# Performance work log

Measured on AMD Instinct MI355X. Metric: run time of the kernel, lower is better.

## Reference

```python
import jax, jax.numpy as jnp
import numpy as np

N, T, E, D, U = 32, 2048, 512, 1024, 256


def setup_inputs() -> dict:
    key = jax.random.key(0)
    ks = jax.random.split(key, 6)
    queries = jax.random.normal(ks[0], (N, 1, D), dtype=jnp.float32)
    prev = jax.random.uniform(ks[1], (N, T), dtype=jnp.float32)
    prev = prev / jnp.sum(prev, axis=1, keepdims=True)  # distribution-like initial alignment
    memory = jax.random.normal(ks[2], (N, T, E), dtype=jnp.float32)
    W_q = jax.random.normal(ks[3], (D, U), dtype=jnp.float32) * (1.0 / np.sqrt(D))
    W_k = jax.random.normal(ks[4], (E, U), dtype=jnp.float32) * (1.0 / np.sqrt(E))
    v = jax.random.uniform(ks[5], (U,), dtype=jnp.float32)
    return {"queries": queries, "previous_alignments": prev, "memory": memory,
            "W_q": W_q, "W_k": W_k, "v": v}


def safe_cumprod_exclusive(x):
    # exclusive cumprod via log-space cumsum, clamped like the torch original
    logsum = jnp.cumsum(jnp.log(jnp.clip(x, 1e-20, 1.0)), axis=1)  # [N,T]
    excl = jnp.concatenate([jnp.zeros_like(logsum[:, :1]), logsum], axis=1)[:, :-1]
    return jnp.exp(excl)


def reference(queries, previous_alignments, memory, W_q, W_k, v):
    # Bahdanau additive score (normalize=False path)
    proj_key = jnp.einsum('bte,eu->btu', memory, W_k)          # set_memory
    proj_q = jnp.einsum('bqd,du->bqu', queries, W_q)           # [N,1,U]
    weights = jnp.einsum('btu,u->bt', jnp.tanh(proj_q + proj_key), v)  # [N,T]
    p_choose = jax.nn.sigmoid(weights)
    # monotonic attention recursion in cumsum/cumprod form
    cumprod_1mp = safe_cumprod_exclusive(1.0 - p_choose)
    alignments = p_choose * cumprod_1mp * jnp.cumsum(
        previous_alignments / jnp.clip(cumprod_1mp, 1e-10, 1.0), axis=1)
    contexts = jnp.einsum('bt,bte->be', alignments, memory)    # bmm + squeeze
    return (contexts, alignments)
```

## Files before the change

kernel.cpp:

```cpp
#include <hip/hip_runtime.h>
#include <math.h>

#define N_ 32
#define T_ 2048
#define E_ 512
#define D_ 1024
#define U_ 256
#define PQ_CH 4

typedef __attribute__((ext_vector_type(8))) short bf16x8;
typedef __attribute__((ext_vector_type(16))) float f32x16;

__device__ __forceinline__ short f2bf_rne(float x) {
  unsigned int u = __float_as_uint(x);
  unsigned int r = u + 0x7FFFu + ((u >> 16) & 1u);
  return (short)(r >> 16);
}
__device__ __forceinline__ float bf2f(short h) {
  return __uint_as_float(((unsigned int)(unsigned short)h) << 16);
}

__global__ __launch_bounds__(256) void wk_convert_kernel(
    const float* __restrict__ Wk, short* __restrict__ whi, short* __restrict__ wlo) {
  __shared__ float tile[64][65];
  const int u0 = blockIdx.x * 64, e0 = blockIdx.y * 64;
  const int tid = threadIdx.x;
  const int c = tid & 63, r4 = tid >> 6;
#pragma unroll
  for (int r = 0; r < 16; ++r) {
    const int e = r * 4 + r4;
    tile[c][e] = Wk[(size_t)(e0 + e) * U_ + u0 + c];
  }
  __syncthreads();
#pragma unroll
  for (int r = 0; r < 16; ++r) {
    const int ul = r * 4 + r4;
    float x = tile[ul][c];
    short h = f2bf_rne(x);
    short l = f2bf_rne(x - bf2f(h));
    whi[(size_t)(u0 + ul) * E_ + e0 + c] = h;
    wlo[(size_t)(u0 + ul) * E_ + e0 + c] = l;
  }
}

__global__ __launch_bounds__(256) void projq_partial_kernel(
    const float* __restrict__ queries, const float* __restrict__ W_q,
    float* __restrict__ pq_part) {
  const int b = blockIdx.y, ch = blockIdx.x, tid = threadIdx.x;
  const int d0 = ch * (D_ / PQ_CH);
  const float* q = queries + b * D_ + d0;
  const float* wq = W_q + (size_t)d0 * U_ + tid;
  float acc = 0.f;
#pragma unroll 8
  for (int d = 0; d < D_ / PQ_CH; ++d)
    acc = fmaf(q[d], wq[(size_t)d * U_], acc);
  pq_part[((b * PQ_CH) + ch) * U_ + tid] = acc;
}

__global__ __launch_bounds__(256) void projq_reduce_kernel(
    const float* __restrict__ pq_part, float* __restrict__ proj_q) {
  const int b = blockIdx.x, tid = threadIdx.x;
  float s = 0.f;
#pragma unroll
  for (int c = 0; c < PQ_CH; ++c) s += pq_part[((b * PQ_CH) + c) * U_ + tid];
  proj_q[b * U_ + tid] = s;
}

__global__ __launch_bounds__(256) void score_kernel(
    const float* __restrict__ memory, const short* __restrict__ whi,
    const short* __restrict__ wlo, const float* __restrict__ proj_q,
    const float* __restrict__ v, float* __restrict__ p_choose) {
  __shared__ short sAhi[2][64 * 64];
  __shared__ short sAlo[2][64 * 64];
  __shared__ float smem_w[4][64];

  const int b = blockIdx.y;
  const int t0 = blockIdx.x * 64;
  const int tid = threadIdx.x;
  const int lane = tid & 63;
  const int ty = tid >> 6;
  const int l31 = lane & 31;
  const int half = lane >> 5;

  f32x16 acc[2][2];
#pragma unroll
  for (int mt = 0; mt < 2; ++mt)
#pragma unroll
    for (int nt = 0; nt < 2; ++nt)
#pragma unroll
      for (int r = 0; r < 16; ++r) acc[mt][nt][r] = 0.f;

  const int sr = tid >> 2;
  const int sc4 = tid & 3;
  const int wslot0 = ((2 * sc4) ^ (sr & 7)) * 16;
  const int wslot1 = ((2 * sc4 + 1) ^ (sr & 7)) * 16;
  const float* srow = memory + ((size_t)(b * T_ + t0 + sr)) * E_ + sc4 * 16;

  float4 xr0, xr1, xr2, xr3;
  auto load_chunk = [&](int it) {
    const float* src = srow + it * 64;
    xr0 = *(const float4*)(src);
    xr1 = *(const float4*)(src + 4);
    xr2 = *(const float4*)(src + 8);
    xr3 = *(const float4*)(src + 12);
  };
  auto stage_chunk = [&](int p) {
    float xs[16] = {xr0.x, xr0.y, xr0.z, xr0.w, xr1.x, xr1.y, xr1.z, xr1.w,
                    xr2.x, xr2.y, xr2.z, xr2.w, xr3.x, xr3.y, xr3.z, xr3.w};
    bf16x8 H0, H1, L0, L1;
#pragma unroll
    for (int i = 0; i < 8; ++i) {
      short h = f2bf_rne(xs[i]);
      H0[i] = h;
      L0[i] = f2bf_rne(xs[i] - bf2f(h));
      short h2 = f2bf_rne(xs[8 + i]);
      H1[i] = h2;
      L1[i] = f2bf_rne(xs[8 + i] - bf2f(h2));
    }
    char* bh = (char*)&sAhi[p][0] + sr * 128;
    char* bl = (char*)&sAlo[p][0] + sr * 128;
    *(bf16x8*)(bh + wslot0) = H0;
    *(bf16x8*)(bh + wslot1) = H1;
    *(bf16x8*)(bl + wslot0) = L0;
    *(bf16x8*)(bl + wslot1) = L1;
  };

  load_chunk(0);
  stage_chunk(0);
  __syncthreads();

  for (int it = 0; it < 8; ++it) {
    const int p = it & 1;
    if (it < 7) load_chunk(it + 1);
    const int e0 = it * 64;
#pragma unroll
    for (int kc = 0; kc < 4; ++kc) {
      bf16x8 bh[2], bl[2];
#pragma unroll
      for (int nt = 0; nt < 2; ++nt) {
        const size_t uo = (size_t)(ty * 64 + nt * 32 + l31) * E_ + e0 + kc * 16 + half * 8;
        bh[nt] = *(const bf16x8*)(whi + uo);
        bl[nt] = *(const bf16x8*)(wlo + uo);
      }
      bf16x8 ah[2], al[2];
#pragma unroll
      for (int mt = 0; mt < 2; ++mt) {
        const int m = mt * 32 + l31;
        const int off = m * 128 + (((kc * 2 + half) ^ (m & 7)) * 16);
        ah[mt] = *(const bf16x8*)((const char*)&sAhi[p][0] + off);
        al[mt] = *(const bf16x8*)((const char*)&sAlo[p][0] + off);
      }
#pragma unroll
      for (int mt = 0; mt < 2; ++mt)
#pragma unroll
        for (int nt = 0; nt < 2; ++nt) {
          acc[mt][nt] = __builtin_amdgcn_mfma_f32_32x32x16_bf16(ah[mt], bh[nt], acc[mt][nt], 0, 0, 0);
          acc[mt][nt] = __builtin_amdgcn_mfma_f32_32x32x16_bf16(ah[mt], bl[nt], acc[mt][nt], 0, 0, 0);
          acc[mt][nt] = __builtin_amdgcn_mfma_f32_32x32x16_bf16(al[mt], bh[nt], acc[mt][nt], 0, 0, 0);
        }
    }
    if (it < 7) {
      stage_chunk(p ^ 1);
      __syncthreads();
    }
  }

  const int u0 = ty * 64 + l31;
  const int u1 = ty * 64 + 32 + l31;
  const float pq0 = proj_q[b * U_ + u0], pq1 = proj_q[b * U_ + u1];
  const float v0 = v[u0], v1 = v[u1];

  float rsum[32];
#pragma unroll
  for (int mt = 0; mt < 2; ++mt)
#pragma unroll
    for (int r = 0; r < 16; ++r)
      rsum[mt * 16 + r] = tanhf(acc[mt][0][r] + pq0) * v0 +
                          tanhf(acc[mt][1][r] + pq1) * v1;
#pragma unroll
  for (int off = 1; off < 32; off <<= 1)
#pragma unroll
    for (int i = 0; i < 32; ++i) rsum[i] += __shfl_xor(rsum[i], off, 64);

  __syncthreads();
  if (l31 == 0) {
#pragma unroll
    for (int mt = 0; mt < 2; ++mt)
#pragma unroll
      for (int r = 0; r < 16; ++r) {
        const int row = mt * 32 + (r & 3) + 8 * (r >> 2) + 4 * half;
        smem_w[ty][row] = rsum[mt * 16 + r];
      }
  }
  __syncthreads();
  if (tid < 64) {
    const float w = smem_w[0][tid] + smem_w[1][tid] + smem_w[2][tid] + smem_w[3][tid];
    p_choose[b * T_ + t0 + tid] = 1.0f / (1.0f + expf(-w));
  }
}

__device__ __forceinline__ float block_incl_scan(float val, float* sbuf, int tid) {
  float x = val;
  sbuf[tid] = x;
  __syncthreads();
#pragma unroll
  for (int off = 1; off < 256; off <<= 1) {
    float t = (tid >= off) ? sbuf[tid - off] : 0.f;
    __syncthreads();
    x += t;
    sbuf[tid] = x;
    __syncthreads();
  }
  return x;
}

__global__ __launch_bounds__(256) void scan_kernel(
    const float* __restrict__ p_choose, const float* __restrict__ prev,
    float* __restrict__ align_out) {
  __shared__ float sbuf[256];
  const int b = blockIdx.x, tid = threadIdx.x;
  const int base = b * T_ + tid * 8;
  float4 p0 = *(const float4*)(p_choose + base);
  float4 p1 = *(const float4*)(p_choose + base + 4);
  float p[8] = {p0.x, p0.y, p0.z, p0.w, p1.x, p1.y, p1.z, p1.w};
  float s[8];
  float run = 0.f;
#pragma unroll
  for (int k = 0; k < 8; ++k) {
    float x = 1.0f - p[k];
    x = fminf(fmaxf(x, 1e-20f), 1.0f);
    run += logf(x);
    s[k] = run;
  }
  float incl = block_incl_scan(run, sbuf, tid);
  float excl = incl - run;
  float cp[8];
#pragma unroll
  for (int k = 0; k < 8; ++k)
    cp[k] = expf(excl + (k ? s[k - 1] : 0.f));
  float4 r0 = *(const float4*)(prev + base);
  float4 r1 = *(const float4*)(prev + base + 4);
  float pr[8] = {r0.x, r0.y, r0.z, r0.w, r1.x, r1.y, r1.z, r1.w};
  float s2[8];
  float run2 = 0.f;
#pragma unroll
  for (int k = 0; k < 8; ++k) {
    float d = fminf(fmaxf(cp[k], 1e-10f), 1.0f);
    run2 += pr[k] / d;
    s2[k] = run2;
  }
  float incl2 = block_incl_scan(run2, sbuf, tid);
  float excl2 = incl2 - run2;
#pragma unroll
  for (int k = 0; k < 8; ++k)
    p[k] = p[k] * cp[k] * (excl2 + s2[k]);
  *(float4*)(align_out + base) = make_float4(p[0], p[1], p[2], p[3]);
  *(float4*)(align_out + base + 4) = make_float4(p[4], p[5], p[6], p[7]);
}

__global__ __launch_bounds__(256) void ctx_partial_kernel(
    const float* __restrict__ memory, const float* __restrict__ align,
    float* __restrict__ partials) {
  const int b = blockIdx.y, ch = blockIdx.x, tid = threadIdx.x;
  const int tg = tid >> 7;
  const int col = (tid & 127) * 4;
  const int t0 = ch * 256 + tg * 128;
  const float* mrow = memory + ((size_t)(b * T_ + t0)) * E_ + col;
  const float* arow = align + b * T_ + t0;
  float4 a = make_float4(0.f, 0.f, 0.f, 0.f);
#pragma unroll 4
  for (int t = 0; t < 128; ++t) {
    float al = arow[t];
    float4 m = *(const float4*)(mrow + (size_t)t * E_);
    a.x = fmaf(al, m.x, a.x);
    a.y = fmaf(al, m.y, a.y);
    a.z = fmaf(al, m.z, a.z);
    a.w = fmaf(al, m.w, a.w);
  }
  *(float4*)(partials + ((size_t)(b * 16 + ch * 2 + tg)) * E_ + col) = a;
}

__global__ __launch_bounds__(256) void ctx_reduce_kernel(
    const float* __restrict__ partials, float* __restrict__ ctx) {
  const int b = blockIdx.x, tid = threadIdx.x;
#pragma unroll
  for (int e = tid; e < E_; e += 256) {
    float s = 0.f;
#pragma unroll
    for (int c = 0; c < 16; ++c) s += partials[((size_t)(b * 16 + c)) * E_ + e];
    ctx[b * E_ + e] = s;
  }
}

extern "C" void kernel_launch(void* const* d_in, const int* in_sizes, int n_in,
                              void* d_out, int out_size, void* d_ws, size_t ws_size,
                              hipStream_t stream) {
  (void)in_sizes; (void)n_in; (void)out_size; (void)ws_size;
  const float* queries = (const float*)d_in[0];
  const float* prev    = (const float*)d_in[1];
  const float* memory  = (const float*)d_in[2];
  const float* W_q     = (const float*)d_in[3];
  const float* W_k     = (const float*)d_in[4];
  const float* v       = (const float*)d_in[5];

  float* out = (float*)d_out;
  float* ctx_out = out;
  float* align_out = out + N_ * E_;

  float* ws = (float*)d_ws;
  short* whi       = (short*)ws;
  short* wlo       = (short*)(ws + 65536);
  float* p_choose  = ws + 131072;
  float* proj_q    = ws + 196608;
  float* pq_part   = ws + 204800;
  float* ctx_parts = ws;

  wk_convert_kernel<<<dim3(U_ / 64, E_ / 64), 256, 0, stream>>>(W_k, whi, wlo);
  projq_partial_kernel<<<dim3(PQ_CH, N_), 256, 0, stream>>>(queries, W_q, pq_part);
  projq_reduce_kernel<<<dim3(N_), 256, 0, stream>>>(pq_part, proj_q);
  score_kernel<<<dim3(T_ / 64, N_), 256, 0, stream>>>(memory, whi, wlo, proj_q, v, p_choose);
  scan_kernel<<<dim3(N_), 256, 0, stream>>>(p_choose, prev, align_out);
  ctx_partial_kernel<<<dim3(8, N_), 256, 0, stream>>>(memory, align_out, ctx_parts);
  ctx_reduce_kernel<<<dim3(N_), 256, 0, stream>>>(ctx_parts, ctx_out);
}
```

Before: 308.5 us.

## Enlarge score tile to 128 rows and pre-pack W_k into MFMA fragment layout

```diff
diff --git a/kernel.cpp b/kernel.cpp
--- a/kernel.cpp
+++ b/kernel.cpp
@@ -16,31 +16,32 @@
   unsigned int r = u + 0x7FFFu + ((u >> 16) & 1u);
   return (short)(r >> 16);
 }
+__device__ __forceinline__ short f2bf_trunc(float x) {
+  return (short)(__float_as_uint(x) >> 16);
+}
 __device__ __forceinline__ float bf2f(short h) {
   return __uint_as_float(((unsigned int)(unsigned short)h) << 16);
 }
 
-__global__ __launch_bounds__(256) void wk_convert_kernel(
-    const float* __restrict__ Wk, short* __restrict__ whi, short* __restrict__ wlo) {
-  __shared__ float tile[64][65];
-  const int u0 = blockIdx.x * 64, e0 = blockIdx.y * 64;
-  const int tid = threadIdx.x;
-  const int c = tid & 63, r4 = tid >> 6;
-#pragma unroll
-  for (int r = 0; r < 16; ++r) {
-    const int e = r * 4 + r4;
-    tile[c][e] = Wk[(size_t)(e0 + e) * U_ + u0 + c];
-  }
-  __syncthreads();
-#pragma unroll
-  for (int r = 0; r < 16; ++r) {
-    const int ul = r * 4 + r4;
-    float x = tile[ul][c];
-    short h = f2bf_rne(x);
-    short l = f2bf_rne(x - bf2f(h));
-    whi[(size_t)(u0 + ul) * E_ + e0 + c] = h;
-    wlo[(size_t)(u0 + ul) * E_ + e0 + c] = l;
-  }
+__global__ __launch_bounds__(256) void wk_pack_kernel(
+    const float* __restrict__ Wk, bf16x8* __restrict__ whiP, bf16x8* __restrict__ wloP) {
+  const int fid = blockIdx.x * 256 + threadIdx.x;
+  const int lane = fid & 63;
+  const int ub = (fid >> 6) & 7;
+  const int kc = (fid >> 9) & 3;
+  const int c = fid >> 11;
+  const int u = ub * 32 + (lane & 31);
+  const int e0 = c * 64 + kc * 16 + (lane >> 5) * 8;
+  bf16x8 H, L;
+#pragma unroll
+  for (int j = 0; j < 8; ++j) {
+    float x = Wk[(size_t)(e0 + j) * U_ + u];
+    short h = f2bf_trunc(x);
+    H[j] = h;
+    L[j] = f2bf_rne(x - bf2f(h));
+  }
+  whiP[fid] = H;
+  wloP[fid] = L;
 }
 
 __global__ __launch_bounds__(256) void projq_partial_kernel(
@@ -66,63 +67,58 @@
   proj_q[b * U_ + tid] = s;
 }
 
-__global__ __launch_bounds__(256) void score_kernel(
-    const float* __restrict__ memory, const short* __restrict__ whi,
-    const short* __restrict__ wlo, const float* __restrict__ proj_q,
+__global__ __launch_bounds__(256, 2) void score_kernel(
+    const float* __restrict__ memory, const bf16x8* __restrict__ whiP,
+    const bf16x8* __restrict__ wloP, const float* __restrict__ proj_q,
     const float* __restrict__ v, float* __restrict__ p_choose) {
-  __shared__ short sAhi[2][64 * 64];
-  __shared__ short sAlo[2][64 * 64];
-  __shared__ float smem_w[4][64];
+  __shared__ short sAhi[2][128 * 64];
+  __shared__ short sAlo[2][128 * 64];
+  __shared__ float smem_w[4][128];
 
   const int b = blockIdx.y;
-  const int t0 = blockIdx.x * 64;
+  const int t0 = blockIdx.x * 128;
   const int tid = threadIdx.x;
   const int lane = tid & 63;
   const int ty = tid >> 6;
   const int l31 = lane & 31;
   const int half = lane >> 5;
 
-  f32x16 acc[2][2];
-#pragma unroll
-  for (int mt = 0; mt < 2; ++mt)
+  f32x16 acc[4][2];
+#pragma unroll
+  for (int mt = 0; mt < 4; ++mt)
 #pragma unroll
     for (int nt = 0; nt < 2; ++nt)
 #pragma unroll
       for (int r = 0; r < 16; ++r) acc[mt][nt][r] = 0.f;
 
-  const int sr = tid >> 2;
-  const int sc4 = tid & 3;
-  const int wslot0 = ((2 * sc4) ^ (sr & 7)) * 16;
-  const int wslot1 = ((2 * sc4 + 1) ^ (sr & 7)) * 16;
-  const float* srow = memory + ((size_t)(b * T_ + t0 + sr)) * E_ + sc4 * 16;
-
-  float4 xr0, xr1, xr2, xr3;
+  const int sr = tid >> 1;
+  const int cs = (tid & 1) * 32;
+  const float* srow = memory + ((size_t)(b * T_ + t0 + sr)) * E_ + cs;
+
+  float4 xr[8];
   auto load_chunk = [&](int it) {
     const float* src = srow + it * 64;
-    xr0 = *(const float4*)(src);
-    xr1 = *(const float4*)(src + 4);
-    xr2 = *(const float4*)(src + 8);
-    xr3 = *(const float4*)(src + 12);
+#pragma unroll
+    for (int j = 0; j < 8; ++j) xr[j] = *(const float4*)(src + j * 4);
   };
   auto stage_chunk = [&](int p) {
-    float xs[16] = {xr0.x, xr0.y, xr0.z, xr0.w, xr1.x, xr1.y, xr1.z, xr1.w,
-                    xr2.x, xr2.y, xr2.z, xr2.w, xr3.x, xr3.y, xr3.z, xr3.w};
-    bf16x8 H0, H1, L0, L1;
-#pragma unroll
-    for (int i = 0; i < 8; ++i) {
-      short h = f2bf_rne(xs[i]);
-      H0[i] = h;
-      L0[i] = f2bf_rne(xs[i] - bf2f(h));
-      short h2 = f2bf_rne(xs[8 + i]);
-      H1[i] = h2;
-      L1[i] = f2bf_rne(xs[8 + i] - bf2f(h2));
-    }
     char* bh = (char*)&sAhi[p][0] + sr * 128;
     char* bl = (char*)&sAlo[p][0] + sr * 128;
-    *(bf16x8*)(bh + wslot0) = H0;
-    *(bf16x8*)(bh + wslot1) = H1;
-    *(bf16x8*)(bl + wslot0) = L0;
-    *(bf16x8*)(bl + wslot1) = L1;
+#pragma unroll
+    for (int j = 0; j < 4; ++j) {
+      float xs[8] = {xr[2 * j].x, xr[2 * j].y, xr[2 * j].z, xr[2 * j].w,
+                     xr[2 * j + 1].x, xr[2 * j + 1].y, xr[2 * j + 1].z, xr[2 * j + 1].w};
+      bf16x8 H, L;
+#pragma unroll
+      for (int i = 0; i < 8; ++i) {
+        short h = f2bf_trunc(xs[i]);
+        H[i] = h;
+        L[i] = f2bf_rne(xs[i] - bf2f(h));
+      }
+      const int slot = (((tid & 1) * 4 + j) ^ (sr & 7)) * 16;
+      *(bf16x8*)(bh + slot) = H;
+      *(bf16x8*)(bl + slot) = L;
+    }
   };
 
   load_chunk(0);
@@ -132,26 +128,25 @@
   for (int it = 0; it < 8; ++it) {
     const int p = it & 1;
     if (it < 7) load_chunk(it + 1);
-    const int e0 = it * 64;
 #pragma unroll
     for (int kc = 0; kc < 4; ++kc) {
       bf16x8 bh[2], bl[2];
 #pragma unroll
       for (int nt = 0; nt < 2; ++nt) {
-        const size_t uo = (size_t)(ty * 64 + nt * 32 + l31) * E_ + e0 + kc * 16 + half * 8;
-        bh[nt] = *(const bf16x8*)(whi + uo);
-        bl[nt] = *(const bf16x8*)(wlo + uo);
+        const int fidx = ((it * 4 + kc) * 8 + (ty * 2 + nt)) * 64 + lane;
+        bh[nt] = whiP[fidx];
+        bl[nt] = wloP[fidx];
       }
-      bf16x8 ah[2], al[2];
-#pragma unroll
-      for (int mt = 0; mt < 2; ++mt) {
+      bf16x8 ah[4], al[4];
+#pragma unroll
+      for (int mt = 0; mt < 4; ++mt) {
         const int m = mt * 32 + l31;
         const int off = m * 128 + (((kc * 2 + half) ^ (m & 7)) * 16);
         ah[mt] = *(const bf16x8*)((const char*)&sAhi[p][0] + off);
         al[mt] = *(const bf16x8*)((const char*)&sAlo[p][0] + off);
       }
 #pragma unroll
-      for (int mt = 0; mt < 2; ++mt)
+      for (int mt = 0; mt < 4; ++mt)
 #pragma unroll
         for (int nt = 0; nt < 2; ++nt) {
           acc[mt][nt] = __builtin_amdgcn_mfma_f32_32x32x16_bf16(ah[mt], bh[nt], acc[mt][nt], 0, 0, 0);
@@ -170,30 +165,20 @@
   const float pq0 = proj_q[b * U_ + u0], pq1 = proj_q[b * U_ + u1];
   const float v0 = v[u0], v1 = v[u1];
 
-  float rsum[32];
-#pragma unroll
-  for (int mt = 0; mt < 2; ++mt)
-#pragma unroll
-    for (int r = 0; r < 16; ++r)
-      rsum[mt * 16 + r] = tanhf(acc[mt][0][r] + pq0) * v0 +
-                          tanhf(acc[mt][1][r] + pq1) * v1;
-#pragma unroll
-  for (int off = 1; off < 32; off <<= 1)
-#pragma unroll
-    for (int i = 0; i < 32; ++i) rsum[i] += __shfl_xor(rsum[i], off, 64);
-
+#pragma unroll
+  for (int mt = 0; mt < 4; ++mt)
+#pragma unroll
+    for (int r = 0; r < 16; ++r) {
+      float s = tanhf(acc[mt][0][r] + pq0) * v0 + tanhf(acc[mt][1][r] + pq1) * v1;
+#pragma unroll
+      for (int off = 1; off < 32; off <<= 1) s += __shfl_xor(s, off, 64);
+      if (l31 == 0) {
+        const int row = mt * 32 + (r & 3) + 8 * (r >> 2) + 4 * half;
+        smem_w[ty][row] = s;
+      }
+    }
   __syncthreads();
-  if (l31 == 0) {
-#pragma unroll
-    for (int mt = 0; mt < 2; ++mt)
-#pragma unroll
-      for (int r = 0; r < 16; ++r) {
-        const int row = mt * 32 + (r & 3) + 8 * (r >> 2) + 4 * half;
-        smem_w[ty][row] = rsum[mt * 16 + r];
-      }
-  }
-  __syncthreads();
-  if (tid < 64) {
+  if (tid < 128) {
     const float w = smem_w[0][tid] + smem_w[1][tid] + smem_w[2][tid] + smem_w[3][tid];
     p_choose[b * T_ + t0 + tid] = 1.0f / (1.0f + expf(-w));
   }
@@ -308,17 +293,17 @@
   float* align_out = out + N_ * E_;
 
   float* ws = (float*)d_ws;
-  short* whi       = (short*)ws;
-  short* wlo       = (short*)(ws + 65536);
+  bf16x8* whiP     = (bf16x8*)ws;
+  bf16x8* wloP     = (bf16x8*)(ws + 65536);
   float* p_choose  = ws + 131072;
   float* proj_q    = ws + 196608;
   float* pq_part   = ws + 204800;
   float* ctx_parts = ws;
 
-  wk_convert_kernel<<<dim3(U_ / 64, E_ / 64), 256, 0, stream>>>(W_k, whi, wlo);
+  wk_pack_kernel<<<dim3(64), 256, 0, stream>>>(W_k, whiP, wloP);
   projq_partial_kernel<<<dim3(PQ_CH, N_), 256, 0, stream>>>(queries, W_q, pq_part);
   projq_reduce_kernel<<<dim3(N_), 256, 0, stream>>>(pq_part, proj_q);
-  score_kernel<<<dim3(T_ / 64, N_), 256, 0, stream>>>(memory, whi, wlo, proj_q, v, p_choose);
+  score_kernel<<<dim3(T_ / 128, N_), 256, 0, stream>>>(memory, whiP, wloP, proj_q, v, p_choose);
   scan_kernel<<<dim3(N_), 256, 0, stream>>>(p_choose, prev, align_out);
   ctx_partial_kernel<<<dim3(8, N_), 256, 0, stream>>>(memory, align_out, ctx_parts);
   ctx_reduce_kernel<<<dim3(N_), 256, 0, stream>>>(ctx_parts, ctx_out);
```

Result: faster. 286.3 us (-7.2%).
